# Kernel optimization log

Measured on AMD Instinct MI355X. Metric: run time of the kernel, lower is better.

Reference implementation:

```python
import jax, jax.numpy as jnp
import numpy as np

B, T, D, H = 4, 2048, 384, 6
HD = D // H  # 64
HALF = HD // 2


def setup_inputs() -> dict:
    key = jax.random.key(0)
    k0, k1, k2 = jax.random.split(key, 3)
    x = jax.random.normal(k0, (B, T, D), jnp.float32)
    attn_bias = jnp.zeros((1, 1, T, T), jnp.float32)  # additive SDPA bias
    # standard RoPE tables: [T, HD/2]
    inv_freq = 1.0 / (10000.0 ** (np.arange(HALF, dtype=np.float32) / HALF))
    ang = np.arange(T, dtype=np.float32)[:, None] * inv_freq[None, :]
    cos = jnp.asarray(np.cos(ang), jnp.float32)
    sin = jnp.asarray(np.sin(ang), jnp.float32)
    w_qkv = jax.random.normal(k1, (D, 3 * D), jnp.float32) * (D ** -0.5)
    w_proj = jax.random.normal(k2, (D, D), jnp.float32) * (D ** -0.5)
    return {"x": x, "attn_bias": attn_bias, "cos": cos, "sin": sin,
            "w_qkv": w_qkv, "w_proj": w_proj}


def _apply_rope(x, cos, sin):
    # x: [b, h, t, hd]; cos/sin: [t, hd/2] -> rotate-half RoPE
    half = x.shape[-1] // 2
    x1, x2 = x[..., :half], x[..., half:]
    c = cos[None, None, :, :]
    s = sin[None, None, :, :]
    return jnp.concatenate([x1 * c - x2 * s, x2 * c + x1 * s], axis=-1)


def reference(x, attn_bias, cos, sin, w_qkv, w_proj):
    b, t, _ = x.shape
    qkv = (x @ w_qkv).reshape(b, t, 3, H, HD)  # fused QKV projection
    q = jnp.transpose(qkv[:, :, 0], (0, 2, 1, 3))  # [b,h,t,hd]
    k = jnp.transpose(qkv[:, :, 1], (0, 2, 1, 3))
    v = jnp.transpose(qkv[:, :, 2], (0, 2, 1, 3))
    q = _apply_rope(q, cos, sin)
    k = _apply_rope(k, cos, sin)
    scale = 1.0 / jnp.sqrt(jnp.asarray(HD, x.dtype))
    scores = jnp.einsum("bhqd,bhkd->bhqk", q, k) * scale + attn_bias
    attn = jax.nn.softmax(scores, axis=-1)
    out = jnp.einsum("bhqk,bhkd->bhqd", attn, v)
    out = jnp.transpose(out, (0, 2, 1, 3)).reshape(b, t, H * HD)
    return out @ w_proj
```

## Files before the change

kernel.cpp:

```cpp
#include <hip/hip_runtime.h>
#include <hip/hip_bf16.h>

#define BB   4
#define TT   2048
#define DDIM 384
#define HH   6
#define HD   64
#define BT   (BB*TT)
#define QKVC (3*DDIM)

#define QSCALE 0.18033688011112042f
#define LOG2E  1.4426950408889634f

typedef __attribute__((ext_vector_type(4))) short short4v;
typedef __attribute__((ext_vector_type(8))) short short8v;
typedef __attribute__((ext_vector_type(4))) float float4v;
typedef unsigned short u16;

static __device__ __forceinline__ u16 f2bu(float f) {
    __hip_bfloat16 h = __float2bfloat16(f);
    return __builtin_bit_cast(u16, h);
}
static __device__ __forceinline__ unsigned pk2(float lo, float hi) {
    return (unsigned)f2bu(lo) | ((unsigned)f2bu(hi) << 16);
}
static __device__ __forceinline__ short8v frag4(uint4 v) {
    return __builtin_bit_cast(short8v, v);
}
static __device__ __forceinline__ short8v ld_frag(const u16* p) {
    short4v a = *(const short4v*)p;
    short4v b = *(const short4v*)(p + 4);
    return __builtin_shufflevector(a, b, 0, 1, 2, 3, 4, 5, 6, 7);
}
static __device__ __forceinline__ void st8(u16* p, uint4 v) {
    *(uint2*)p       = make_uint2(v.x, v.y);
    *(uint2*)(p + 4) = make_uint2(v.z, v.w);
}
static __device__ __forceinline__ void pl32swap(unsigned &a, unsigned &b) {
    auto r = __builtin_amdgcn_permlane32_swap(a, b, false, false);
    a = r[0]; b = r[1];
}
static __device__ __forceinline__ void pl16swap(unsigned &a, unsigned &b) {
    auto r = __builtin_amdgcn_permlane16_swap(a, b, false, false);
    a = r[0]; b = r[1];
}

#define MFMA16(a, b, c) __builtin_amdgcn_mfma_f32_16x16x32_bf16((a), (b), (c), 0, 0, 0)

static __device__ __forceinline__ void stage_wT(
    u16 (*ws)[392], const float* __restrict__ w, int C, int c0, int t)
{
    const int c = t & 63;
    const int kb0 = t >> 6;
    #pragma unroll
    for (int u = 0; u < 12; ++u) {
        int k = (kb0 + 4 * u) * 8;
        const float* wp = w + (size_t)k * C + c0 + c;
        float v0 = wp[0];
        float v1 = wp[(size_t)1 * C];
        float v2 = wp[(size_t)2 * C];
        float v3 = wp[(size_t)3 * C];
        float v4 = wp[(size_t)4 * C];
        float v5 = wp[(size_t)5 * C];
        float v6 = wp[(size_t)6 * C];
        float v7 = wp[(size_t)7 * C];
        uint4 pv = make_uint4(pk2(v0, v1), pk2(v2, v3), pk2(v4, v5), pk2(v6, v7));
        *(uint4*)&ws[c][k] = pv;
    }
}

__global__ __launch_bounds__(256, 3) void qkv_fused_kernel(
    const float* __restrict__ x, const float* __restrict__ wqkv,
    const float* __restrict__ bias,
    const float* __restrict__ cs, const float* __restrict__ sn,
    u16* __restrict__ qb, u16* __restrict__ kb, u16* __restrict__ vtb,
    unsigned* __restrict__ flag)
{
    const int bid = blockIdx.x;
    const int t = threadIdx.x;
    if (bid >= 2304) {
        const float* gp = bias + (size_t)(bid - 2304) * 4096 + (size_t)t * 16;
        unsigned acc = 0;
        #pragma unroll
        for (int u = 0; u < 4; ++u) {
            float4 v = *(const float4*)(gp + 4 * u);
            acc |= (__builtin_bit_cast(unsigned, v.x) & 0x7fffffffu);
            acc |= (__builtin_bit_cast(unsigned, v.y) & 0x7fffffffu);
            acc |= (__builtin_bit_cast(unsigned, v.z) & 0x7fffffffu);
            acc |= (__builtin_bit_cast(unsigned, v.w) & 0x7fffffffu);
        }
        if (acc) atomicOr(flag, 1u);
        return;
    }

    __shared__ __align__(16) u16 ws[64][392];
    const int wv = t >> 6, lane = t & 63, quad = lane >> 4, lo = lane & 15;
    const int c0 = (bid % 18) * 64;
    const int r0 = (bid / 18) * 64;

    stage_wT(ws, wqkv, QKVC, c0, t);

    const float* arow = x + (size_t)(r0 + 16 * wv + lo) * DDIM + quad * 8;
    uint4 af[12];
    #pragma unroll
    for (int kf = 0; kf < 12; ++kf) {
        float4 a0 = *(const float4*)(arow + kf * 32);
        float4 a1 = *(const float4*)(arow + kf * 32 + 4);
        af[kf] = make_uint4(pk2(a0.x, a0.y), pk2(a0.z, a0.w),
                            pk2(a1.x, a1.y), pk2(a1.z, a1.w));
    }
    __syncthreads();

    float4v acc[4] = {};
    #pragma unroll
    for (int kf = 0; kf < 12; ++kf) {
        short8v a = frag4(af[kf]);
        #pragma unroll
        for (int nt = 0; nt < 4; ++nt) {
            short8v b = ld_frag(&ws[nt * 16 + lo][kf * 32 + quad * 8]);
            acc[nt] = MFMA16(a, b, acc[nt]);
        }
    }

    const int cb = bid % 18;
    const int sec = cb / 6;
    const int h   = cb % 6;
    const int rbase = r0 + 16 * wv + 4 * quad;
    const int bidx  = r0 >> 11;
    const int tbase = rbase & (TT - 1);

    if (sec == 2) {
        #pragma unroll
        for (int nt = 0; nt < 4; ++nt) {
            int d = nt * 16 + lo;
            unsigned a0 = pk2(acc[nt][0], acc[nt][1]);
            unsigned a1 = pk2(acc[nt][2], acc[nt][3]);
            u16* gp = vtb + ((size_t)(bidx * HH + h) * HD + d) * TT + tbase;
            *(uint2*)gp = make_uint2(a0, a1);
        }
    } else {
        u16* dst = (sec == 0) ? qb : kb;
        const float scl = (sec == 0) ? QSCALE : 1.0f;
        #pragma unroll
        for (int np = 0; np < 2; ++np) {
            #pragma unroll
            for (int r = 0; r < 4; ++r) {
                int tpos = tbase + r;
                int ci = np * 16 + lo;
                float cv = cs[tpos * 32 + ci];
                float sv = sn[tpos * 32 + ci];
                float x1 = acc[np][r], x2 = acc[np + 2][r];
                u16* gp = dst + ((size_t)(bidx * HH + h) * TT + tpos) * HD;
                gp[ci]      = f2bu((x1 * cv - x2 * sv) * scl);
                gp[ci + 32] = f2bu((x2 * cv + x1 * sv) * scl);
            }
        }
    }
}

__global__ __launch_bounds__(256, 2) void attn_unified_kernel(
    const u16* __restrict__ qb, const u16* __restrict__ kb, const u16* __restrict__ vtb,
    const float* __restrict__ bias, const unsigned* __restrict__ flag,
    u16* __restrict__ ob)
{
    __shared__ __align__(16) u16 smem[17920];

    const int t = threadIdx.x;
    const int wv = t >> 6, lane = t & 63, quad = lane >> 4, lo = lane & 15;
    const int bh = blockIdx.x;
    const int b = bh / HH, h = bh % HH;
    const int q0 = blockIdx.y * 64;

    if (*flag == 0u) {
        float* red_o = (float*)smem;
        float* red_l = (float*)(smem + 17408);

        short8v aq[4][2];
        #pragma unroll
        for (int g = 0; g < 4; ++g) {
            const u16* qp = qb + ((size_t)bh * TT + q0 + g * 16 + lo) * HD + quad * 8;
            aq[g][0] = frag4(*(const uint4*)qp);
            aq[g][1] = frag4(*(const uint4*)(qp + 32));
        }

        const u16* kbase = kb + ((size_t)bh * TT + lo) * HD + quad * 8;
        const u16* vbase = vtb + ((size_t)bh * HD + lo) * TT + quad * 8;

        uint4 kq[4][2], vq[4][2];
        {
            const size_t ko = (size_t)wv * 64 * HD;
            const size_t vo = (size_t)wv * 64;
            #pragma unroll
            for (int nt = 0; nt < 4; ++nt) {
                kq[nt][0] = *(const uint4*)(kbase + ko + (size_t)nt * 16 * HD);
                kq[nt][1] = *(const uint4*)(kbase + ko + (size_t)nt * 16 * HD + 32);
            }
            #pragma unroll
            for (int dt = 0; dt < 4; ++dt) {
                vq[dt][0] = *(const uint4*)(vbase + (size_t)dt * 16 * TT + vo);
                vq[dt][1] = *(const uint4*)(vbase + (size_t)dt * 16 * TT + vo + 32);
            }
        }

        float4v oacc[4][4] = {};
        float lacc[4] = {0.f, 0.f, 0.f, 0.f};

        for (int j = 0; j < 8; ++j) {
            const int ktn = (j < 7) ? (wv + 4 * (j + 1)) : wv;
            const size_t kno = (size_t)ktn * 64 * HD;
            const size_t vno = (size_t)ktn * 64;

            #pragma unroll
            for (int g = 0; g < 4; ++g) {
                float4v s[4] = {};
                #pragma unroll
                for (int nt = 0; nt < 4; ++nt)
                    s[nt] = MFMA16(frag4(kq[nt][0]), aq[g][0], s[nt]);
                #pragma unroll
                for (int nt = 0; nt < 4; ++nt)
                    s[nt] = MFMA16(frag4(kq[nt][1]), aq[g][1], s[nt]);
                if (g == 3) {
                    #pragma unroll
                    for (int nt = 0; nt < 4; ++nt) {
                        kq[nt][0] = *(const uint4*)(kbase + kno + (size_t)nt * 16 * HD);
                        kq[nt][1] = *(const uint4*)(kbase + kno + (size_t)nt * 16 * HD + 32);
                    }
                }

                unsigned w[8];
                #pragma unroll
                for (int nt = 0; nt < 4; ++nt) {
                    float p0 = __builtin_amdgcn_exp2f(s[nt][0]);
                    float p1 = __builtin_amdgcn_exp2f(s[nt][1]);
                    float p2 = __builtin_amdgcn_exp2f(s[nt][2]);
                    float p3 = __builtin_amdgcn_exp2f(s[nt][3]);
                    lacc[g] += (p0 + p1) + (p2 + p3);
                    w[2 * nt]     = pk2(p0, p1);
                    w[2 * nt + 1] = pk2(p2, p3);
                }

                pl32swap(w[0], w[2]); pl16swap(w[0], w[2]);
                pl32swap(w[1], w[3]); pl16swap(w[1], w[3]);
                pl32swap(w[4], w[6]); pl16swap(w[4], w[6]);
                pl32swap(w[5], w[7]); pl16swap(w[5], w[7]);
                short8v pa0 = frag4(make_uint4(w[0], w[1], w[2], w[3]));
                short8v pa1 = frag4(make_uint4(w[4], w[5], w[6], w[7]));

                #pragma unroll
                for (int dt = 0; dt < 4; ++dt)
                    oacc[g][dt] = MFMA16(pa0, frag4(vq[dt][0]), oacc[g][dt]);
                #pragma unroll
                for (int dt = 0; dt < 4; ++dt)
                    oacc[g][dt] = MFMA16(pa1, frag4(vq[dt][1]), oacc[g][dt]);
                if (g == 3) {
                    #pragma unroll
                    for (int dt = 0; dt < 4; ++dt) {
                        vq[dt][0] = *(const uint4*)(vbase + (size_t)dt * 16 * TT + vno);
                        vq[dt][1] = *(const uint4*)(vbase + (size_t)dt * 16 * TT + vno + 32);
                    }
                }
            }
        }

        #pragma unroll
        for (int g = 0; g < 4; ++g) {
            lacc[g] += __shfl_xor(lacc[g], 16);
            lacc[g] += __shfl_xor(lacc[g], 32);
        }
        if (quad == 0) {
            #pragma unroll
            for (int g = 0; g < 4; ++g) red_l[wv * 64 + g * 16 + lo] = lacc[g];
        }
        float* slot0 = red_o + (size_t)lane * 68;
        float* slot1 = red_o + 64 * 68 + (size_t)lane * 68;
        if (wv == 1 || wv == 3) {
            float* sp = (wv == 1) ? slot0 : slot1;
            #pragma unroll
            for (int g = 0; g < 4; ++g)
                #pragma unroll
                for (int dt = 0; dt < 4; ++dt)
                    *(float4v*)(sp + (g * 4 + dt) * 4) = oacc[g][dt];
        }
        __syncthreads();
        if (wv == 0 || wv == 2) {
            float* sp = (wv == 0) ? slot0 : slot1;
            #pragma unroll
            for (int g = 0; g < 4; ++g)
                #pragma unroll
                for (int dt = 0; dt < 4; ++dt)
                    oacc[g][dt] += *(const float4v*)(sp + (g * 4 + dt) * 4);
        }
        __syncthreads();
        if (wv == 2) {
            #pragma unroll
            for (int g = 0; g < 4; ++g)
                #pragma unroll
                for (int dt = 0; dt < 4; ++dt)
                    *(float4v*)(slot1 + (g * 4 + dt) * 4) = oacc[g][dt];
        }
        __syncthreads();
        if (wv == 0) {
            #pragma unroll
            for (int g = 0; g < 4; ++g) {
                #pragma unroll
                for (int dt = 0; dt < 4; ++dt)
                    oacc[g][dt] += *(const float4v*)(slot1 + (g * 4 + dt) * 4);
                float lt = red_l[0 * 64 + g * 16 + lo] + red_l[1 * 64 + g * 16 + lo]
                         + red_l[2 * 64 + g * 16 + lo] + red_l[3 * 64 + g * 16 + lo];
                #pragma unroll
                for (int r = 0; r < 4; ++r) {
                    float lr = __shfl(lt, 4 * quad + r);
                    float inv = 1.f / lr;
                    u16* gp = ob + ((size_t)b * TT + q0 + g * 16 + 4 * quad + r) * DDIM
                                 + h * HD + lo;
                    #pragma unroll
                    for (int dt = 0; dt < 4; ++dt)
                        gp[dt * 16] = f2bu(oacc[g][dt][r] * inv);
                }
            }
        }
        return;
    }

    {
        typedef u16 (*lds_t)[64][68];
        lds_t ks = (lds_t)smem;
        lds_t vt = (lds_t)(smem + 8704);

        const int qrow = q0 + 16 * wv + lo;
        const u16* qbase = qb + ((size_t)bh * TT + qrow) * HD + quad * 8;
        short8v aq0 = frag4(*(const uint4*)qbase);
        short8v aq1 = frag4(*(const uint4*)(qbase + 32));

        const int sr = t >> 3, sd = (t & 7) * 8;
        const u16* kbbase = kb + (size_t)bh * TT * HD;
        const u16* vtbase = vtb + (size_t)bh * HD * TT;
        const float* brow = bias + (size_t)qrow * TT + 4 * quad;

        st8(&ks[0][sr][sd],      *(const uint4*)(kbbase + (size_t)sr * HD + sd));
        st8(&ks[0][sr + 32][sd], *(const uint4*)(kbbase + (size_t)(sr + 32) * HD + sd));
        st8(&vt[0][sr][sd],      *(const uint4*)(vtbase + (size_t)sr * TT + sd));
        st8(&vt[0][sr + 32][sd], *(const uint4*)(vtbase + (size_t)(sr + 32) * TT + sd));
        float4 bcur[4];
        #pragma unroll
        for (int nt = 0; nt < 4; ++nt) bcur[nt] = *(const float4*)(brow + nt * 16);
        __syncthreads();

        float4v oacc[4] = {};
        float lacc[4] = {0.f, 0.f, 0.f, 0.f};

        for (int kt = 0; kt < TT / 64; ++kt) {
            const int cur = kt & 1, nxt = cur ^ 1;
            const int kn = (kt < 31 ? kt + 1 : 31) * 64;

            uint4 kp0 = *(const uint4*)(kbbase + (size_t)(kn + sr) * HD + sd);
            uint4 kp1 = *(const uint4*)(kbbase + (size_t)(kn + sr + 32) * HD + sd);
            uint4 vp0 = *(const uint4*)(vtbase + (size_t)sr * TT + kn + sd);
            uint4 vp1 = *(const uint4*)(vtbase + (size_t)(sr + 32) * TT + kn + sd);
            float4 bnxt[4];
            #pragma unroll
            for (int nt = 0; nt < 4; ++nt)
                bnxt[nt] = *(const float4*)(brow + kn + nt * 16);

            float4v s[4] = {};
            #pragma unroll
            for (int kf = 0; kf < 2; ++kf) {
                #pragma unroll
                for (int nt = 0; nt < 4; ++nt) {
                    short8v kfr = ld_frag(&ks[cur][nt * 16 + lo][kf * 32 + quad * 8]);
                    s[nt] = MFMA16(kfr, (kf ? aq1 : aq0), s[nt]);
                }
            }

            unsigned w[8];
            #pragma unroll
            for (int nt = 0; nt < 4; ++nt) {
                float p0 = __builtin_amdgcn_exp2f(fmaf(bcur[nt].x, LOG2E, s[nt][0]));
                float p1 = __builtin_amdgcn_exp2f(fmaf(bcur[nt].y, LOG2E, s[nt][1]));
                float p2 = __builtin_amdgcn_exp2f(fmaf(bcur[nt].z, LOG2E, s[nt][2]));
                float p3 = __builtin_amdgcn_exp2f(fmaf(bcur[nt].w, LOG2E, s[nt][3]));
                lacc[nt] += (p0 + p1) + (p2 + p3);
                w[2 * nt]     = pk2(p0, p1);
                w[2 * nt + 1] = pk2(p2, p3);
            }

            pl32swap(w[0], w[2]); pl16swap(w[0], w[2]);
            pl32swap(w[1], w[3]); pl16swap(w[1], w[3]);
            pl32swap(w[4], w[6]); pl16swap(w[4], w[6]);
            pl32swap(w[5], w[7]); pl16swap(w[5], w[7]);
            short8v pa0 = frag4(make_uint4(w[0], w[1], w[2], w[3]));
            short8v pa1 = frag4(make_uint4(w[4], w[5], w[6], w[7]));

            #pragma unroll
            for (int kf = 0; kf < 2; ++kf) {
                #pragma unroll
                for (int dt = 0; dt < 4; ++dt) {
                    short8v bv = ld_frag(&vt[cur][dt * 16 + lo][kf * 32 + quad * 8]);
                    oacc[dt] = MFMA16((kf ? pa1 : pa0), bv, oacc[dt]);
                }
            }

            st8(&ks[nxt][sr][sd], kp0);
            st8(&ks[nxt][sr + 32][sd], kp1);
            st8(&vt[nxt][sr][sd], vp0);
            st8(&vt[nxt][sr + 32][sd], vp1);
            #pragma unroll
            for (int nt = 0; nt < 4; ++nt) bcur[nt] = bnxt[nt];
            __syncthreads();
        }

        float l = (lacc[0] + lacc[1]) + (lacc[2] + lacc[3]);
        l += __shfl_xor(l, 16);
        l += __shfl_xor(l, 32);
        #pragma unroll
        for (int r = 0; r < 4; ++r) {
            float lr = __shfl(l, 4 * quad + r);
            float inv = 1.f / lr;
            u16* gp = ob + ((size_t)b * TT + q0 + 16 * wv + 4 * quad + r) * DDIM
                         + h * HD + lo;
            #pragma unroll
            for (int dt = 0; dt < 4; ++dt)
                gp[dt * 16] = f2bu(oacc[dt][r] * inv);
        }
    }
}

__global__ __launch_bounds__(256, 3) void proj_fused_kernel(
    const u16* __restrict__ o, const float* __restrict__ wproj,
    float* __restrict__ out)
{
    __shared__ __align__(16) u16 ws[64][392];
    const int t = threadIdx.x;
    const int wv = t >> 6, lane = t & 63, quad = lane >> 4, lo = lane & 15;
    const int r0 = blockIdx.y * 64, c0 = blockIdx.x * 64;

    stage_wT(ws, wproj, DDIM, c0, t);

    const u16* arow = o + (size_t)(r0 + 16 * wv + lo) * DDIM + quad * 8;
    uint4 af[12];
    #pragma unroll
    for (int kf = 0; kf < 12; ++kf)
        af[kf] = *(const uint4*)(arow + kf * 32);
    __syncthreads();

    float4v acc[4] = {};
    #pragma unroll
    for (int kf = 0; kf < 12; ++kf) {
        short8v a = frag4(af[kf]);
        #pragma unroll
        for (int nt = 0; nt < 4; ++nt) {
            short8v b = ld_frag(&ws[nt * 16 + lo][kf * 32 + quad * 8]);
            acc[nt] = MFMA16(a, b, acc[nt]);
        }
    }
    #pragma unroll
    for (int r = 0; r < 4; ++r) {
        float* gp = out + (size_t)(r0 + 16 * wv + 4 * quad + r) * DDIM + c0;
        #pragma unroll
        for (int nt = 0; nt < 4; ++nt)
            gp[nt * 16 + lo] = acc[nt][r];
    }
}

extern "C" void kernel_launch(void* const* d_in, const int* in_sizes, int n_in,
                              void* d_out, int out_size, void* d_ws, size_t ws_size,
                              hipStream_t stream) {
    const float* x     = (const float*)d_in[0];
    const float* bias  = (const float*)d_in[1];
    const float* cs    = (const float*)d_in[2];
    const float* sn    = (const float*)d_in[3];
    const float* wqkv  = (const float*)d_in[4];
    const float* wproj = (const float*)d_in[5];
    float* out = (float*)d_out;

    u16* qb  = (u16*)d_ws;
    u16* kb  = qb + (size_t)BB * HH * TT * HD;
    u16* vtb = kb + (size_t)BB * HH * TT * HD;
    u16* ob  = vtb + (size_t)BB * HH * TT * HD;
    unsigned* flag = (unsigned*)(ob + (size_t)BT * DDIM);

    hipMemsetAsync(flag, 0, sizeof(unsigned), stream);
    qkv_fused_kernel<<<2304 + TT * TT / 4096, 256, 0, stream>>>(
        x, wqkv, bias, cs, sn, qb, kb, vtb, flag);
    attn_unified_kernel<<<dim3(BB * HH, TT / 64), 256, 0, stream>>>(
        qb, kb, vtb, bias, flag, ob);
    proj_fused_kernel<<<dim3(DDIM / 64, BT / 64), 256, 0, stream>>>(
        ob, wproj, out);
}
```

Measured before the change: 177.6 us.

## Fuse QKV, attention and projection into one persistent kernel with grid barriers

Replaces the three separate launches (QKV+RoPE, attention, output projection) with a single persistent kernel of 768 blocks. The blocks loop over the bias-check and QKV tiles, wait at a software grid barrier built on atomics, run one attention tile each, and then do the projection after a second barrier. The aim is to remove launch gaps and kernel tail effects between stages. The cost is spin-wait barrier overhead, and the barrier needs all 768 blocks to be co-resident, which depends on occupancy with the larger shared-memory footprint and the three-blocks-per-SM launch bound.

```diff
diff --git a/kernel.cpp b/kernel.cpp
--- a/kernel.cpp
+++ b/kernel.cpp
@@ -8,6 +8,7 @@
 #define HD   64
 #define BT   (BB*TT)
 #define QKVC (3*DDIM)
+#define NBLK 768
 
 #define QSCALE 0.18033688011112042f
 #define LOG2E  1.4426950408889634f
@@ -46,6 +47,19 @@
 }
 
 #define MFMA16(a, b, c) __builtin_amdgcn_mfma_f32_16x16x32_bf16((a), (b), (c), 0, 0, 0)
+
+static __device__ __forceinline__ void grid_barrier(unsigned* bar, int t) {
+    __syncthreads();
+    if (t == 0) {
+        __hip_atomic_fetch_add(bar, 1u, __ATOMIC_ACQ_REL, __HIP_MEMORY_SCOPE_AGENT);
+        unsigned v;
+        do {
+            __builtin_amdgcn_s_sleep(2);
+            v = __hip_atomic_load(bar, __ATOMIC_ACQUIRE, __HIP_MEMORY_SCOPE_AGENT);
+        } while (v < NBLK);
+    }
+    __syncthreads();
+}
 
 static __device__ __forceinline__ void stage_wT(
     u16 (*ws)[392], const float* __restrict__ w, int C, int c0, int t)
@@ -69,172 +83,313 @@
     }
 }
 
-__global__ __launch_bounds__(256, 3) void qkv_fused_kernel(
+__global__ __launch_bounds__(256, 3) void fused_mhsa_kernel(
     const float* __restrict__ x, const float* __restrict__ wqkv,
-    const float* __restrict__ bias,
+    const float* __restrict__ wproj, const float* __restrict__ bias,
     const float* __restrict__ cs, const float* __restrict__ sn,
     u16* __restrict__ qb, u16* __restrict__ kb, u16* __restrict__ vtb,
-    unsigned* __restrict__ flag)
+    u16* __restrict__ ob, float* __restrict__ out,
+    unsigned* __restrict__ sync)
 {
-    const int bid = blockIdx.x;
+    __shared__ __align__(16) u16 smem[25088];
     const int t = threadIdx.x;
-    if (bid >= 2304) {
-        const float* gp = bias + (size_t)(bid - 2304) * 4096 + (size_t)t * 16;
-        unsigned acc = 0;
+    const int blk = blockIdx.x;
+    const int wv = t >> 6, lane = t & 63, quad = lane >> 4, lo = lane & 15;
+
+    for (int it = blk; it < 3328; it += NBLK) {
+        if (it < 1024) {
+            const float* gp = bias + (size_t)it * 4096 + (size_t)t * 16;
+            unsigned acc = 0;
+            #pragma unroll
+            for (int u = 0; u < 4; ++u) {
+                float4 v = *(const float4*)(gp + 4 * u);
+                acc |= (__builtin_bit_cast(unsigned, v.x) & 0x7fffffffu);
+                acc |= (__builtin_bit_cast(unsigned, v.y) & 0x7fffffffu);
+                acc |= (__builtin_bit_cast(unsigned, v.z) & 0x7fffffffu);
+                acc |= (__builtin_bit_cast(unsigned, v.w) & 0x7fffffffu);
+            }
+            if (acc) atomicOr(sync, 1u);
+            continue;
+        }
+        const int qid = it - 1024;
+        const int c0 = (qid % 18) * 64;
+        const int r0 = (qid / 18) * 64;
+        u16 (*ws)[392] = (u16(*)[392])smem;
+
+        __syncthreads();
+        stage_wT(ws, wqkv, QKVC, c0, t);
+
+        const float* arow = x + (size_t)(r0 + 16 * wv + lo) * DDIM + quad * 8;
+        uint4 af[12];
         #pragma unroll
-        for (int u = 0; u < 4; ++u) {
-            float4 v = *(const float4*)(gp + 4 * u);
-            acc |= (__builtin_bit_cast(unsigned, v.x) & 0x7fffffffu);
-            acc |= (__builtin_bit_cast(unsigned, v.y) & 0x7fffffffu);
-            acc |= (__builtin_bit_cast(unsigned, v.z) & 0x7fffffffu);
-            acc |= (__builtin_bit_cast(unsigned, v.w) & 0x7fffffffu);
-        }
-        if (acc) atomicOr(flag, 1u);
-        return;
+        for (int kf = 0; kf < 12; ++kf) {
+            float4 a0 = *(const float4*)(arow + kf * 32);
+            float4 a1 = *(const float4*)(arow + kf * 32 + 4);
+            af[kf] = make_uint4(pk2(a0.x, a0.y), pk2(a0.z, a0.w),
+                                pk2(a1.x, a1.y), pk2(a1.z, a1.w));
+        }
+        __syncthreads();
+
+        float4v acc[4] = {};
+        #pragma unroll
+        for (int kf = 0; kf < 12; ++kf) {
+            short8v a = frag4(af[kf]);
+            #pragma unroll
+            for (int nt = 0; nt < 4; ++nt) {
+                short8v b = ld_frag(&ws[nt * 16 + lo][kf * 32 + quad * 8]);
+                acc[nt] = MFMA16(a, b, acc[nt]);
+            }
+        }
+
+        const int cb = qid % 18;
+        const int sec = cb / 6;
+        const int h   = cb % 6;
+        const int rbase = r0 + 16 * wv + 4 * quad;
+        const int bidx  = r0 >> 11;
+        const int tbase = rbase & (TT - 1);
+
+        if (sec == 2) {
+            #pragma unroll
+            for (int nt = 0; nt < 4; ++nt) {
+                int d = nt * 16 + lo;
+                unsigned a0 = pk2(acc[nt][0], acc[nt][1]);
+                unsigned a1 = pk2(acc[nt][2], acc[nt][3]);
+                u16* gp = vtb + ((size_t)(bidx * HH + h) * HD + d) * TT + tbase;
+                *(uint2*)gp = make_uint2(a0, a1);
+            }
+        } else {
+            u16* dst = (sec == 0) ? qb : kb;
+            const float scl = (sec == 0) ? QSCALE : 1.0f;
+            #pragma unroll
+            for (int np = 0; np < 2; ++np) {
+                #pragma unroll
+                for (int r = 0; r < 4; ++r) {
+                    int tpos = tbase + r;
+                    int ci = np * 16 + lo;
+                    float cv = cs[tpos * 32 + ci];
+                    float sv = sn[tpos * 32 + ci];
+                    float x1 = acc[np][r], x2 = acc[np + 2][r];
+                    u16* gp = dst + ((size_t)(bidx * HH + h) * TT + tpos) * HD;
+                    gp[ci]      = f2bu((x1 * cv - x2 * sv) * scl);
+                    gp[ci + 32] = f2bu((x2 * cv + x1 * sv) * scl);
+                }
+            }
+        }
     }
 
-    __shared__ __align__(16) u16 ws[64][392];
-    const int wv = t >> 6, lane = t & 63, quad = lane >> 4, lo = lane & 15;
-    const int c0 = (bid % 18) * 64;
-    const int r0 = (bid / 18) * 64;
-
-    stage_wT(ws, wqkv, QKVC, c0, t);
-
-    const float* arow = x + (size_t)(r0 + 16 * wv + lo) * DDIM + quad * 8;
-    uint4 af[12];
-    #pragma unroll
-    for (int kf = 0; kf < 12; ++kf) {
-        float4 a0 = *(const float4*)(arow + kf * 32);
-        float4 a1 = *(const float4*)(arow + kf * 32 + 4);
-        af[kf] = make_uint4(pk2(a0.x, a0.y), pk2(a0.z, a0.w),
-                            pk2(a1.x, a1.y), pk2(a1.z, a1.w));
-    }
-    __syncthreads();
-
-    float4v acc[4] = {};
-    #pragma unroll
-    for (int kf = 0; kf < 12; ++kf) {
-        short8v a = frag4(af[kf]);
-        #pragma unroll
-        for (int nt = 0; nt < 4; ++nt) {
-            short8v b = ld_frag(&ws[nt * 16 + lo][kf * 32 + quad * 8]);
-            acc[nt] = MFMA16(a, b, acc[nt]);
-        }
-    }
-
-    const int cb = bid % 18;
-    const int sec = cb / 6;
-    const int h   = cb % 6;
-    const int rbase = r0 + 16 * wv + 4 * quad;
-    const int bidx  = r0 >> 11;
-    const int tbase = rbase & (TT - 1);
-
-    if (sec == 2) {
-        #pragma unroll
-        for (int nt = 0; nt < 4; ++nt) {
-            int d = nt * 16 + lo;
-            unsigned a0 = pk2(acc[nt][0], acc[nt][1]);
-            unsigned a1 = pk2(acc[nt][2], acc[nt][3]);
-            u16* gp = vtb + ((size_t)(bidx * HH + h) * HD + d) * TT + tbase;
-            *(uint2*)gp = make_uint2(a0, a1);
-        }
-    } else {
-        u16* dst = (sec == 0) ? qb : kb;
-        const float scl = (sec == 0) ? QSCALE : 1.0f;
-        #pragma unroll
-        for (int np = 0; np < 2; ++np) {
-            #pragma unroll
-            for (int r = 0; r < 4; ++r) {
-                int tpos = tbase + r;
-                int ci = np * 16 + lo;
-                float cv = cs[tpos * 32 + ci];
-                float sv = sn[tpos * 32 + ci];
-                float x1 = acc[np][r], x2 = acc[np + 2][r];
-                u16* gp = dst + ((size_t)(bidx * HH + h) * TT + tpos) * HD;
-                gp[ci]      = f2bu((x1 * cv - x2 * sv) * scl);
-                gp[ci + 32] = f2bu((x2 * cv + x1 * sv) * scl);
-            }
-        }
-    }
-}
-
-__global__ __launch_bounds__(256, 2) void attn_unified_kernel(
-    const u16* __restrict__ qb, const u16* __restrict__ kb, const u16* __restrict__ vtb,
-    const float* __restrict__ bias, const unsigned* __restrict__ flag,
-    u16* __restrict__ ob)
-{
-    __shared__ __align__(16) u16 smem[17920];
-
-    const int t = threadIdx.x;
-    const int wv = t >> 6, lane = t & 63, quad = lane >> 4, lo = lane & 15;
-    const int bh = blockIdx.x;
-    const int b = bh / HH, h = bh % HH;
-    const int q0 = blockIdx.y * 64;
-
-    if (*flag == 0u) {
-        float* red_o = (float*)smem;
-        float* red_l = (float*)(smem + 17408);
-
-        short8v aq[4][2];
-        #pragma unroll
-        for (int g = 0; g < 4; ++g) {
-            const u16* qp = qb + ((size_t)bh * TT + q0 + g * 16 + lo) * HD + quad * 8;
-            aq[g][0] = frag4(*(const uint4*)qp);
-            aq[g][1] = frag4(*(const uint4*)(qp + 32));
-        }
-
-        const u16* kbase = kb + ((size_t)bh * TT + lo) * HD + quad * 8;
-        const u16* vbase = vtb + ((size_t)bh * HD + lo) * TT + quad * 8;
-
-        uint4 kq[4][2], vq[4][2];
-        {
-            const size_t ko = (size_t)wv * 64 * HD;
-            const size_t vo = (size_t)wv * 64;
-            #pragma unroll
-            for (int nt = 0; nt < 4; ++nt) {
-                kq[nt][0] = *(const uint4*)(kbase + ko + (size_t)nt * 16 * HD);
-                kq[nt][1] = *(const uint4*)(kbase + ko + (size_t)nt * 16 * HD + 32);
-            }
-            #pragma unroll
-            for (int dt = 0; dt < 4; ++dt) {
-                vq[dt][0] = *(const uint4*)(vbase + (size_t)dt * 16 * TT + vo);
-                vq[dt][1] = *(const uint4*)(vbase + (size_t)dt * 16 * TT + vo + 32);
-            }
-        }
-
-        float4v oacc[4][4] = {};
-        float lacc[4] = {0.f, 0.f, 0.f, 0.f};
-
-        for (int j = 0; j < 8; ++j) {
-            const int ktn = (j < 7) ? (wv + 4 * (j + 1)) : wv;
-            const size_t kno = (size_t)ktn * 64 * HD;
-            const size_t vno = (size_t)ktn * 64;
-
+    grid_barrier(sync + 1, t);
+
+    {
+        const int bh = blk % 24;
+        const int b = bh / HH, h = bh % HH;
+        const int q0 = (blk / 24) * 64;
+
+        if (sync[0] == 0u) {
+            float* red_o = (float*)smem;
+            float* red_l = (float*)(smem + 17408);
+
+            short8v aq[4][2];
             #pragma unroll
             for (int g = 0; g < 4; ++g) {
+                const u16* qp = qb + ((size_t)bh * TT + q0 + g * 16 + lo) * HD + quad * 8;
+                aq[g][0] = frag4(*(const uint4*)qp);
+                aq[g][1] = frag4(*(const uint4*)(qp + 32));
+            }
+
+            const u16* kbase = kb + ((size_t)bh * TT + lo) * HD + quad * 8;
+            const u16* vbase = vtb + ((size_t)bh * HD + lo) * TT + quad * 8;
+
+            uint4 kq[4][2], vq[4][2];
+            {
+                const size_t ko = (size_t)wv * 64 * HD;
+                const size_t vo = (size_t)wv * 64;
+                #pragma unroll
+                for (int nt = 0; nt < 4; ++nt) {
+                    kq[nt][0] = *(const uint4*)(kbase + ko + (size_t)nt * 16 * HD);
+                    kq[nt][1] = *(const uint4*)(kbase + ko + (size_t)nt * 16 * HD + 32);
+                }
+                #pragma unroll
+                for (int dt = 0; dt < 4; ++dt) {
+                    vq[dt][0] = *(const uint4*)(vbase + (size_t)dt * 16 * TT + vo);
+                    vq[dt][1] = *(const uint4*)(vbase + (size_t)dt * 16 * TT + vo + 32);
+                }
+            }
+
+            float4v oacc[4][4] = {};
+            float lacc[4] = {0.f, 0.f, 0.f, 0.f};
+
+            for (int j = 0; j < 8; ++j) {
+                const int ktn = (j < 7) ? (wv + 4 * (j + 1)) : wv;
+                const size_t kno = (size_t)ktn * 64 * HD;
+                const size_t vno = (size_t)ktn * 64;
+
+                #pragma unroll
+                for (int g = 0; g < 4; ++g) {
+                    float4v s[4] = {};
+                    #pragma unroll
+                    for (int nt = 0; nt < 4; ++nt)
+                        s[nt] = MFMA16(frag4(kq[nt][0]), aq[g][0], s[nt]);
+                    #pragma unroll
+                    for (int nt = 0; nt < 4; ++nt)
+                        s[nt] = MFMA16(frag4(kq[nt][1]), aq[g][1], s[nt]);
+                    if (g == 3) {
+                        #pragma unroll
+                        for (int nt = 0; nt < 4; ++nt) {
+                            kq[nt][0] = *(const uint4*)(kbase + kno + (size_t)nt * 16 * HD);
+                            kq[nt][1] = *(const uint4*)(kbase + kno + (size_t)nt * 16 * HD + 32);
+                        }
+                    }
+
+                    unsigned w[8];
+                    #pragma unroll
+                    for (int nt = 0; nt < 4; ++nt) {
+                        float p0 = __builtin_amdgcn_exp2f(s[nt][0]);
+                        float p1 = __builtin_amdgcn_exp2f(s[nt][1]);
+                        float p2 = __builtin_amdgcn_exp2f(s[nt][2]);
+                        float p3 = __builtin_amdgcn_exp2f(s[nt][3]);
+                        lacc[g] += (p0 + p1) + (p2 + p3);
+                        w[2 * nt]     = pk2(p0, p1);
+                        w[2 * nt + 1] = pk2(p2, p3);
+                    }
+
+                    pl32swap(w[0], w[2]); pl16swap(w[0], w[2]);
+                    pl32swap(w[1], w[3]); pl16swap(w[1], w[3]);
+                    pl32swap(w[4], w[6]); pl16swap(w[4], w[6]);
+                    pl32swap(w[5], w[7]); pl16swap(w[5], w[7]);
+                    short8v pa0 = frag4(make_uint4(w[0], w[1], w[2], w[3]));
+                    short8v pa1 = frag4(make_uint4(w[4], w[5], w[6], w[7]));
+
+                    #pragma unroll
+                    for (int dt = 0; dt < 4; ++dt)
+                        oacc[g][dt] = MFMA16(pa0, frag4(vq[dt][0]), oacc[g][dt]);
+                    #pragma unroll
+                    for (int dt = 0; dt < 4; ++dt)
+                        oacc[g][dt] = MFMA16(pa1, frag4(vq[dt][1]), oacc[g][dt]);
+                    if (g == 3) {
+                        #pragma unroll
+                        for (int dt = 0; dt < 4; ++dt) {
+                            vq[dt][0] = *(const uint4*)(vbase + (size_t)dt * 16 * TT + vno);
+                            vq[dt][1] = *(const uint4*)(vbase + (size_t)dt * 16 * TT + vno + 32);
+                        }
+                    }
+                }
+            }
+
+            #pragma unroll
+            for (int g = 0; g < 4; ++g) {
+                lacc[g] += __shfl_xor(lacc[g], 16);
+                lacc[g] += __shfl_xor(lacc[g], 32);
+            }
+            if (quad == 0) {
+                #pragma unroll
+                for (int g = 0; g < 4; ++g) red_l[wv * 64 + g * 16 + lo] = lacc[g];
+            }
+            float* slot0 = red_o + (size_t)lane * 68;
+            float* slot1 = red_o + 64 * 68 + (size_t)lane * 68;
+            if (wv == 1 || wv == 3) {
+                float* sp = (wv == 1) ? slot0 : slot1;
+                #pragma unroll
+                for (int g = 0; g < 4; ++g)
+                    #pragma unroll
+                    for (int dt = 0; dt < 4; ++dt)
+                        *(float4v*)(sp + (g * 4 + dt) * 4) = oacc[g][dt];
+            }
+            __syncthreads();
+            if (wv == 0 || wv == 2) {
+                float* sp = (wv == 0) ? slot0 : slot1;
+                #pragma unroll
+                for (int g = 0; g < 4; ++g)
+                    #pragma unroll
+                    for (int dt = 0; dt < 4; ++dt)
+                        oacc[g][dt] += *(const float4v*)(sp + (g * 4 + dt) * 4);
+            }
+            __syncthreads();
+            if (wv == 2) {
+                #pragma unroll
+                for (int g = 0; g < 4; ++g)
+                    #pragma unroll
+                    for (int dt = 0; dt < 4; ++dt)
+                        *(float4v*)(slot1 + (g * 4 + dt) * 4) = oacc[g][dt];
+            }
+            __syncthreads();
+            if (wv == 0) {
+                #pragma unroll
+                for (int g = 0; g < 4; ++g) {
+                    #pragma unroll
+                    for (int dt = 0; dt < 4; ++dt)
+                        oacc[g][dt] += *(const float4v*)(slot1 + (g * 4 + dt) * 4);
+                    float lt = red_l[0 * 64 + g * 16 + lo] + red_l[1 * 64 + g * 16 + lo]
+                             + red_l[2 * 64 + g * 16 + lo] + red_l[3 * 64 + g * 16 + lo];
+                    #pragma unroll
+                    for (int r = 0; r < 4; ++r) {
+                        float lr = __shfl(lt, 4 * quad + r);
+                        float inv = 1.f / lr;
+                        u16* gp = ob + ((size_t)b * TT + q0 + g * 16 + 4 * quad + r) * DDIM
+                                     + h * HD + lo;
+                        #pragma unroll
+                        for (int dt = 0; dt < 4; ++dt)
+                            gp[dt * 16] = f2bu(oacc[g][dt][r] * inv);
+                    }
+                }
+            }
+        } else {
+            typedef u16 (*lds_t)[64][68];
+            lds_t ks = (lds_t)smem;
+            lds_t vt = (lds_t)(smem + 8704);
+
+            const int qrow = q0 + 16 * wv + lo;
+            const u16* qbase = qb + ((size_t)bh * TT + qrow) * HD + quad * 8;
+            short8v aq0 = frag4(*(const uint4*)qbase);
+            short8v aq1 = frag4(*(const uint4*)(qbase + 32));
+
+            const int sr = t >> 3, sd = (t & 7) * 8;
+            const u16* kbbase = kb + (size_t)bh * TT * HD;
+            const u16* vtbase = vtb + (size_t)bh * HD * TT;
+            const float* brow = bias + (size_t)qrow * TT + 4 * quad;
+
+            st8(&ks[0][sr][sd],      *(const uint4*)(kbbase + (size_t)sr * HD + sd));
+            st8(&ks[0][sr + 32][sd], *(const uint4*)(kbbase + (size_t)(sr + 32) * HD + sd));
+            st8(&vt[0][sr][sd],      *(const uint4*)(vtbase + (size_t)sr * TT + sd));
+            st8(&vt[0][sr + 32][sd], *(const uint4*)(vtbase + (size_t)(sr + 32) * TT + sd));
+            float4 bcur[4];
+            #pragma unroll
+            for (int nt = 0; nt < 4; ++nt) bcur[nt] = *(const float4*)(brow + nt * 16);
+            __syncthreads();
+
+            float4v oacc[4] = {};
+            float lacc[4] = {0.f, 0.f, 0.f, 0.f};
+
+            for (int kt = 0; kt < TT / 64; ++kt) {
+                const int cur = kt & 1, nxt = cur ^ 1;
+                const int kn = (kt < 31 ? kt + 1 : 31) * 64;
+
+                uint4 kp0 = *(const uint4*)(kbbase + (size_t)(kn + sr) * HD + sd);
+                uint4 kp1 = *(const uint4*)(kbbase + (size_t)(kn + sr + 32) * HD + sd);
+                uint4 vp0 = *(const uint4*)(vtbase + (size_t)sr * TT + kn + sd);
+                uint4 vp1 = *(const uint4*)(vtbase + (size_t)(sr + 32) * TT + kn + sd);
+                float4 bnxt[4];
+                #pragma unroll
+                for (int nt = 0; nt < 4; ++nt)
+                    bnxt[nt] = *(const float4*)(brow + kn + nt * 16);
+
                 float4v s[4] = {};
                 #pragma unroll
-                for (int nt = 0; nt < 4; ++nt)
-                    s[nt] = MFMA16(frag4(kq[nt][0]), aq[g][0], s[nt]);
-                #pragma unroll
-                for (int nt = 0; nt < 4; ++nt)
-                    s[nt] = MFMA16(frag4(kq[nt][1]), aq[g][1], s[nt]);
-                if (g == 3) {
+                for (int kf = 0; kf < 2; ++kf) {
                     #pragma unroll
                     for (int nt = 0; nt < 4; ++nt) {
-                        kq[nt][0] = *(const uint4*)(kbase + kno + (size_t)nt * 16 * HD);
-                        kq[nt][1] = *(const uint4*)(kbase + kno + (size_t)nt * 16 * HD + 32);
+                        short8v kfr = ld_frag(&ks[cur][nt * 16 + lo][kf * 32 + quad * 8]);
+                        s[nt] = MFMA16(kfr, (kf ? aq1 : aq0), s[nt]);
                     }
                 }
 
                 unsigned w[8];
                 #pragma unroll
                 for (int nt = 0; nt < 4; ++nt) {
-                    float p0 = __builtin_amdgcn_exp2f(s[nt][0]);
-                    float p1 = __builtin_amdgcn_exp2f(s[nt][1]);
-                    float p2 = __builtin_amdgcn_exp2f(s[nt][2]);
-                    float p3 = __builtin_amdgcn_exp2f(s[nt][3]);
-                    lacc[g] += (p0 + p1) + (p2 + p3);
+                    float p0 = __builtin_amdgcn_exp2f(fmaf(bcur[nt].x, LOG2E, s[nt][0]));
+                    float p1 = __builtin_amdgcn_exp2f(fmaf(bcur[nt].y, LOG2E, s[nt][1]));
+                    float p2 = __builtin_amdgcn_exp2f(fmaf(bcur[nt].z, LOG2E, s[nt][2]));
+                    float p3 = __builtin_amdgcn_exp2f(fmaf(bcur[nt].w, LOG2E, s[nt][3]));
+                    lacc[nt] += (p0 + p1) + (p2 + p3);
                     w[2 * nt]     = pk2(p0, p1);
                     w[2 * nt + 1] = pk2(p2, p3);
                 }
@@ -247,218 +402,72 @@
                 short8v pa1 = frag4(make_uint4(w[4], w[5], w[6], w[7]));
 
                 #pragma unroll
+                for (int kf = 0; kf < 2; ++kf) {
+                    #pragma unroll
+                    for (int dt = 0; dt < 4; ++dt) {
+                        short8v bv = ld_frag(&vt[cur][dt * 16 + lo][kf * 32 + quad * 8]);
+                        oacc[dt] = MFMA16((kf ? pa1 : pa0), bv, oacc[dt]);
+                    }
+                }
+
+                st8(&ks[nxt][sr][sd], kp0);
+                st8(&ks[nxt][sr + 32][sd], kp1);
+                st8(&vt[nxt][sr][sd], vp0);
+                st8(&vt[nxt][sr + 32][sd], vp1);
+                #pragma unroll
+                for (int nt = 0; nt < 4; ++nt) bcur[nt] = bnxt[nt];
+                __syncthreads();
+            }
+
+            float l = (lacc[0] + lacc[1]) + (lacc[2] + lacc[3]);
+            l += __shfl_xor(l, 16);
+            l += __shfl_xor(l, 32);
+            #pragma unroll
+            for (int r = 0; r < 4; ++r) {
+                float lr = __shfl(l, 4 * quad + r);
+                float inv = 1.f / lr;
+                u16* gp = ob + ((size_t)b * TT + q0 + 16 * wv + 4 * quad + r) * DDIM
+                             + h * HD + lo;
+                #pragma unroll
                 for (int dt = 0; dt < 4; ++dt)
-                    oacc[g][dt] = MFMA16(pa0, frag4(vq[dt][0]), oacc[g][dt]);
-                #pragma unroll
-                for (int dt = 0; dt < 4; ++dt)
-                    oacc[g][dt] = MFMA16(pa1, frag4(vq[dt][1]), oacc[g][dt]);
-                if (g == 3) {
-                    #pragma unroll
-                    for (int dt = 0; dt < 4; ++dt) {
-                        vq[dt][0] = *(const uint4*)(vbase + (size_t)dt * 16 * TT + vno);
-                        vq[dt][1] = *(const uint4*)(vbase + (size_t)dt * 16 * TT + vno + 32);
-                    }
-                }
-            }
-        }
-
+                    gp[dt * 16] = f2bu(oacc[dt][r] * inv);
+            }
+        }
+    }
+
+    grid_barrier(sync + 2, t);
+
+    {
+        const int c0 = (blk % 6) * 64;
+        const int r0 = (blk / 6) * 64;
+        u16 (*ws)[392] = (u16(*)[392])smem;
+
+        stage_wT(ws, wproj, DDIM, c0, t);
+
+        const u16* arow = ob + (size_t)(r0 + 16 * wv + lo) * DDIM + quad * 8;
+        uint4 af[12];
         #pragma unroll
-        for (int g = 0; g < 4; ++g) {
-            lacc[g] += __shfl_xor(lacc[g], 16);
-            lacc[g] += __shfl_xor(lacc[g], 32);
-        }
-        if (quad == 0) {
-            #pragma unroll
-            for (int g = 0; g < 4; ++g) red_l[wv * 64 + g * 16 + lo] = lacc[g];
-        }
-        float* slot0 = red_o + (size_t)lane * 68;
-        float* slot1 = red_o + 64 * 68 + (size_t)lane * 68;
-        if (wv == 1 || wv == 3) {
-            float* sp = (wv == 1) ? slot0 : slot1;
-            #pragma unroll
-            for (int g = 0; g < 4; ++g)
-                #pragma unroll
-                for (int dt = 0; dt < 4; ++dt)
-                    *(float4v*)(sp + (g * 4 + dt) * 4) = oacc[g][dt];
-        }
+        for (int kf = 0; kf < 12; ++kf)
+            af[kf] = *(const uint4*)(arow + kf * 32);
         __syncthreads();
-        if (wv == 0 || wv == 2) {
-            float* sp = (wv == 0) ? slot0 : slot1;
-            #pragma unroll
-            for (int g = 0; g < 4; ++g)
-                #pragma unroll
-                for (int dt = 0; dt < 4; ++dt)
-                    oacc[g][dt] += *(const float4v*)(sp + (g * 4 + dt) * 4);
-        }
-        __syncthreads();
-        if (wv == 2) {
-            #pragma unroll
-            for (int g = 0; g < 4; ++g)
-                #pragma unroll
-                for (int dt = 0; dt < 4; ++dt)
-                    *(float4v*)(slot1 + (g * 4 + dt) * 4) = oacc[g][dt];
-        }
-        __syncthreads();
-        if (wv == 0) {
-            #pragma unroll
-            for (int g = 0; g < 4; ++g) {
-                #pragma unroll
-                for (int dt = 0; dt < 4; ++dt)
-                    oacc[g][dt] += *(const float4v*)(slot1 + (g * 4 + dt) * 4);
-                float lt = red_l[0 * 64 + g * 16 + lo] + red_l[1 * 64 + g * 16 + lo]
-                         + red_l[2 * 64 + g * 16 + lo] + red_l[3 * 64 + g * 16 + lo];
-                #pragma unroll
-                for (int r = 0; r < 4; ++r) {
-                    float lr = __shfl(lt, 4 * quad + r);
-                    float inv = 1.f / lr;
-                    u16* gp = ob + ((size_t)b * TT + q0 + g * 16 + 4 * quad + r) * DDIM
-                                 + h * HD + lo;
-                    #pragma unroll
-                    for (int dt = 0; dt < 4; ++dt)
-                        gp[dt * 16] = f2bu(oacc[g][dt][r] * inv);
-                }
-            }
-        }
-        return;
-    }
-
-    {
-        typedef u16 (*lds_t)[64][68];
-        lds_t ks = (lds_t)smem;
-        lds_t vt = (lds_t)(smem + 8704);
-
-        const int qrow = q0 + 16 * wv + lo;
-        const u16* qbase = qb + ((size_t)bh * TT + qrow) * HD + quad * 8;
-        short8v aq0 = frag4(*(const uint4*)qbase);
-        short8v aq1 = frag4(*(const uint4*)(qbase + 32));
-
-        const int sr = t >> 3, sd = (t & 7) * 8;
-        const u16* kbbase = kb + (size_t)bh * TT * HD;
-        const u16* vtbase = vtb + (size_t)bh * HD * TT;
-        const float* brow = bias + (size_t)qrow * TT + 4 * quad;
-
-        st8(&ks[0][sr][sd],      *(const uint4*)(kbbase + (size_t)sr * HD + sd));
-        st8(&ks[0][sr + 32][sd], *(const uint4*)(kbbase + (size_t)(sr + 32) * HD + sd));
-        st8(&vt[0][sr][sd],      *(const uint4*)(vtbase + (size_t)sr * TT + sd));
-        st8(&vt[0][sr + 32][sd], *(const uint4*)(vtbase + (size_t)(sr + 32) * TT + sd));
-        float4 bcur[4];
+
+        float4v acc[4] = {};
         #pragma unroll
-        for (int nt = 0; nt < 4; ++nt) bcur[nt] = *(const float4*)(brow + nt * 16);
-        __syncthreads();
-
-        float4v oacc[4] = {};
-        float lacc[4] = {0.f, 0.f, 0.f, 0.f};
-
-        for (int kt = 0; kt < TT / 64; ++kt) {
-            const int cur = kt & 1, nxt = cur ^ 1;
-            const int kn = (kt < 31 ? kt + 1 : 31) * 64;
-
-            uint4 kp0 = *(const uint4*)(kbbase + (size_t)(kn + sr) * HD + sd);
-            uint4 kp1 = *(const uint4*)(kbbase + (size_t)(kn + sr + 32) * HD + sd);
-            uint4 vp0 = *(const uint4*)(vtbase + (size_t)sr * TT + kn + sd);
-            uint4 vp1 = *(const uint4*)(vtbase + (size_t)(sr + 32) * TT + kn + sd);
-            float4 bnxt[4];
-            #pragma unroll
-            for (int nt = 0; nt < 4; ++nt)
-                bnxt[nt] = *(const float4*)(brow + kn + nt * 16);
-
-            float4v s[4] = {};
-            #pragma unroll
-            for (int kf = 0; kf < 2; ++kf) {
-                #pragma unroll
-                for (int nt = 0; nt < 4; ++nt) {
-                    short8v kfr = ld_frag(&ks[cur][nt * 16 + lo][kf * 32 + quad * 8]);
-                    s[nt] = MFMA16(kfr, (kf ? aq1 : aq0), s[nt]);
-                }
-            }
-
-            unsigned w[8];
+        for (int kf = 0; kf < 12; ++kf) {
+            short8v a = frag4(af[kf]);
             #pragma unroll
             for (int nt = 0; nt < 4; ++nt) {
-                float p0 = __builtin_amdgcn_exp2f(fmaf(bcur[nt].x, LOG2E, s[nt][0]));
-                float p1 = __builtin_amdgcn_exp2f(fmaf(bcur[nt].y, LOG2E, s[nt][1]));
-                float p2 = __builtin_amdgcn_exp2f(fmaf(bcur[nt].z, LOG2E, s[nt][2]));
-                float p3 = __builtin_amdgcn_exp2f(fmaf(bcur[nt].w, LOG2E, s[nt][3]));
-                lacc[nt] += (p0 + p1) + (p2 + p3);
-                w[2 * nt]     = pk2(p0, p1);
-                w[2 * nt + 1] = pk2(p2, p3);
-            }
-
-            pl32swap(w[0], w[2]); pl16swap(w[0], w[2]);
-            pl32swap(w[1], w[3]); pl16swap(w[1], w[3]);
-            pl32swap(w[4], w[6]); pl16swap(w[4], w[6]);
-            pl32swap(w[5], w[7]); pl16swap(w[5], w[7]);
-            short8v pa0 = frag4(make_uint4(w[0], w[1], w[2], w[3]));
-            short8v pa1 = frag4(make_uint4(w[4], w[5], w[6], w[7]));
-
-            #pragma unroll
-            for (int kf = 0; kf < 2; ++kf) {
-                #pragma unroll
-                for (int dt = 0; dt < 4; ++dt) {
-                    short8v bv = ld_frag(&vt[cur][dt * 16 + lo][kf * 32 + quad * 8]);
-                    oacc[dt] = MFMA16((kf ? pa1 : pa0), bv, oacc[dt]);
-                }
-            }
-
-            st8(&ks[nxt][sr][sd], kp0);
-            st8(&ks[nxt][sr + 32][sd], kp1);
-            st8(&vt[nxt][sr][sd], vp0);
-            st8(&vt[nxt][sr + 32][sd], vp1);
-            #pragma unroll
-            for (int nt = 0; nt < 4; ++nt) bcur[nt] = bnxt[nt];
-            __syncthreads();
-        }
-
-        float l = (lacc[0] + lacc[1]) + (lacc[2] + lacc[3]);
-        l += __shfl_xor(l, 16);
-        l += __shfl_xor(l, 32);
+                short8v b = ld_frag(&ws[nt * 16 + lo][kf * 32 + quad * 8]);
+                acc[nt] = MFMA16(a, b, acc[nt]);
+            }
+        }
         #pragma unroll
         for (int r = 0; r < 4; ++r) {
-            float lr = __shfl(l, 4 * quad + r);
-            float inv = 1.f / lr;
-            u16* gp = ob + ((size_t)b * TT + q0 + 16 * wv + 4 * quad + r) * DDIM
-                         + h * HD + lo;
-            #pragma unroll
-            for (int dt = 0; dt < 4; ++dt)
-                gp[dt * 16] = f2bu(oacc[dt][r] * inv);
-        }
-    }
-}
-
-__global__ __launch_bounds__(256, 3) void proj_fused_kernel(
-    const u16* __restrict__ o, const float* __restrict__ wproj,
-    float* __restrict__ out)
-{
-    __shared__ __align__(16) u16 ws[64][392];
-    const int t = threadIdx.x;
-    const int wv = t >> 6, lane = t & 63, quad = lane >> 4, lo = lane & 15;
-    const int r0 = blockIdx.y * 64, c0 = blockIdx.x * 64;
-
-    stage_wT(ws, wproj, DDIM, c0, t);
-
-    const u16* arow = o + (size_t)(r0 + 16 * wv + lo) * DDIM + quad * 8;
-    uint4 af[12];
-    #pragma unroll
-    for (int kf = 0; kf < 12; ++kf)
-        af[kf] = *(const uint4*)(arow + kf * 32);
-    __syncthreads();
-
-    float4v acc[4] = {};
-    #pragma unroll
-    for (int kf = 0; kf < 12; ++kf) {
-        short8v a = frag4(af[kf]);
-        #pragma unroll
-        for (int nt = 0; nt < 4; ++nt) {
-            short8v b = ld_frag(&ws[nt * 16 + lo][kf * 32 + quad * 8]);
-            acc[nt] = MFMA16(a, b, acc[nt]);
-        }
-    }
-    #pragma unroll
-    for (int r = 0; r < 4; ++r) {
-        float* gp = out + (size_t)(r0 + 16 * wv + 4 * quad + r) * DDIM + c0;
-        #pragma unroll
-        for (int nt = 0; nt < 4; ++nt)
-            gp[nt * 16 + lo] = acc[nt][r];
+            float* gp = out + (size_t)(r0 + 16 * wv + 4 * quad + r) * DDIM + c0;
+            #pragma unroll
+            for (int nt = 0; nt < 4; ++nt)
+                gp[nt * 16 + lo] = acc[nt][r];
+        }
     }
 }
 
@@ -477,13 +486,9 @@
     u16* kb  = qb + (size_t)BB * HH * TT * HD;
     u16* vtb = kb + (size_t)BB * HH * TT * HD;
     u16* ob  = vtb + (size_t)BB * HH * TT * HD;
-    unsigned* flag = (unsigned*)(ob + (size_t)BT * DDIM);
-
-    hipMemsetAsync(flag, 0, sizeof(unsigned), stream);
-    qkv_fused_kernel<<<2304 + TT * TT / 4096, 256, 0, stream>>>(
-        x, wqkv, bias, cs, sn, qb, kb, vtb, flag);
-    attn_unified_kernel<<<dim3(BB * HH, TT / 64), 256, 0, stream>>>(
-        qb, kb, vtb, bias, flag, ob);
-    proj_fused_kernel<<<dim3(DDIM / 64, BT / 64), 256, 0, stream>>>(
-        ob, wproj, out);
-}
+    unsigned* sync = (unsigned*)(ob + (size_t)BT * DDIM);
+
+    hipMemsetAsync(sync, 0, 3 * sizeof(unsigned), stream);
+    fused_mhsa_kernel<<<NBLK, 256, 0, stream>>>(
+        x, wqkv, wproj, bias, cs, sn, qb, kb, vtb, ob, out, sync);
+}
```

Result: slower. 599.6 us (+237.7%).
